# Kernel tuning notes

Measured on AMD Instinct MI355X. Metric: run time of the kernel, lower is better.

The kernel has to match this reference:

```python
import jax, jax.numpy as jnp
import numpy as np

N_NODES = 10000
N_EDGES = 640000
F_DIM = 128


def setup_inputs() -> dict:
    key = jax.random.key(0)
    k1, k2, k3, k4, k5 = jax.random.split(key, 5)
    x = jax.random.normal(k1, (N_NODES, F_DIM), dtype=jnp.float32)
    W = jax.random.uniform(k2, (F_DIM,), dtype=jnp.float32)
    edge_weight = jax.random.uniform(k3, (N_EDGES,), dtype=jnp.float32)
    edge_src = jax.random.randint(k4, (N_EDGES,), 0, N_NODES, dtype=jnp.int32)
    edge_dst = jax.random.randint(k5, (N_EDGES,), 0, N_NODES, dtype=jnp.int32)
    return {"x": x, "W": W, "edge_weight": edge_weight,
            "edge_src": edge_src, "edge_dst": edge_dst}


def reference(x, W, edge_weight, edge_src, edge_dst):
    # x @ diag(W) is just an elementwise column scale (no FxF materialization)
    xs = x * W[None, :]                                  # [N, F]
    # adj @ xs with adj given as a weighted edge list:
    # out[d] = sum_{e: dst[e]=d} edge_weight[e] * xs[src[e]]
    msgs = xs[edge_src] * edge_weight[:, None]           # [E, F] gather-scale
    out = jax.ops.segment_sum(msgs, edge_dst, num_segments=N_NODES)  # [N, F]
    return out
```

## Files before the change

### kernel.cpp

```cpp
#include <hip/hip_runtime.h>


#define F_DIM 128
#define NB 256
#define TILE 4096
#define SORT_T 512
#define NT_MAX 512
#define NH_MAX 32
#define CAPC 160

__device__ __forceinline__ unsigned f2bf_bits(float f)
{
    unsigned u = __float_as_uint(f);
    return (u + 0x7FFFu + ((u >> 16) & 1u)) >> 16;
}

__global__ void __launch_bounds__(SORT_T)
conv_sort1_kernel(const float* __restrict__ x, const float* __restrict__ W,
                  unsigned* __restrict__ xb,
                  const int* __restrict__ src, const int* __restrict__ dst,
                  const float* __restrict__ ew,
                  unsigned* __restrict__ tab, uint2* __restrict__ segs,
                  int NU4, int NT, int E, unsigned M, int R)
{
    __shared__ unsigned reo_lo[TILE];
    __shared__ unsigned reo_hi[TILE];
    __shared__ int hist[NB], scn[NB], wsum[8];

    int tid = threadIdx.x;

    if ((int)blockIdx.x >= NT) {
        int t = ((int)blockIdx.x - NT) * SORT_T + tid;
        if (t < NU4) {
            int n = t >> 4, jq = t & 15;
            const float4* xr = (const float4*)(x + (size_t)n * F_DIM + jq * 4);
            float4 a  = xr[0];
            float4 bb = xr[16];
            const float4* wr = (const float4*)(W + jq * 4);
            float4 wa = wr[0], wb = wr[16];
            uint4 o;
            o.x = f2bf_bits(a.x * wa.x) | (f2bf_bits(bb.x * wb.x) << 16);
            o.y = f2bf_bits(a.y * wa.y) | (f2bf_bits(bb.y * wb.y) << 16);
            o.z = f2bf_bits(a.z * wa.z) | (f2bf_bits(bb.z * wb.z) << 16);
            o.w = f2bf_bits(a.w * wa.w) | (f2bf_bits(bb.w * wb.w) << 16);
            *(uint4*)(xb + (size_t)n * 64 + jq * 4) = o;
        }
        return;
    }

    int tile  = (int)blockIdx.x;
    int tile0 = tile * TILE;
    int tcnt  = E - tile0; if (tcnt > TILE) tcnt = TILE;

    if (tid < NB) hist[tid] = 0;
    __syncthreads();

    int b_k[8], rank_k[8]; unsigned lo_k[8], w_k[8];
    #pragma unroll
    for (int k = 0; k < 8; ++k) {
        int e = tile0 + k * SORT_T + tid;
        b_k[k] = -1; rank_k[k] = 0; lo_k[k] = 0; w_k[k] = 0;
        if (e < E) {
            int d = dst[e];
            int b = (int)__umulhi((unsigned)d, M);
            int dl = d - b * R;
            b_k[k]    = b;
            lo_k[k]   = ((unsigned)src[e] & 0x3FFFu) | ((unsigned)dl << 14)
                      | ((unsigned)b << 21);
            w_k[k]    = __float_as_uint(ew[e]);
            rank_k[k] = atomicAdd(&hist[b], 1);
        }
    }
    __syncthreads();

    {
        int lane6 = tid & 63, wv = tid >> 6;
        int v = (tid < NB) ? hist[tid] : 0;
        #pragma unroll
        for (int d = 1; d < 64; d <<= 1) {
            int t2 = __shfl_up(v, d);
            if (lane6 >= d) v += t2;
        }
        if (lane6 == 63) wsum[wv] = v;
        __syncthreads();
        if (tid < NB) {
            int woff = 0;
            #pragma unroll
            for (int i2 = 0; i2 < 4; ++i2) if (i2 < wv) woff += wsum[i2];
            scn[tid] = v + woff;
        }
        __syncthreads();
    }

    #pragma unroll
    for (int k = 0; k < 8; ++k) {
        if (b_k[k] >= 0) {
            int b = b_k[k];
            int pos = (scn[b] - hist[b]) + rank_k[k];
            reo_lo[pos] = lo_k[k];
            reo_hi[pos] = w_k[k];
        }
    }
    __syncthreads();

    if (tid < NB)
        tab[(size_t)tid * NT_MAX + tile] =
            ((unsigned)(scn[tid] - hist[tid]) << 16) | (unsigned)hist[tid];

    for (int p = tid; p < tcnt; p += SORT_T)
        segs[(size_t)tile * TILE + p] = make_uint2(reo_lo[p], reo_hi[p]);
}

__global__ void __launch_bounds__(512)
bucket_kernel(const unsigned* __restrict__ xb, const unsigned* __restrict__ tab,
              const uint2* __restrict__ segs, float* __restrict__ out,
              int N, int R, int NT)
{
    __shared__ __align__(16) float          w_l[NH_MAX * CAPC];
    __shared__ __align__(16) unsigned short s_l[NH_MAX * CAPC];
    __shared__ unsigned tabrow[NT_MAX];
    __shared__ int cur[NH_MAX];
    __shared__ int ovf_flag;

    int blk = blockIdx.x;
    int b   = blk >> 1;
    int jh  = blk & 1;
    int tid = threadIdx.x;

    int NHALF = (R + 1) >> 1;
    int brow0 = b * R;
    int rows  = N - brow0; if (rows > R) rows = R;
    if (rows <= 0) return;
    int nlo = jh * NHALF;
    int nh  = rows - nlo; if (nh > NHALF) nh = NHALF;
    if (nh <= 0) return;

    for (int t = tid; t < NT; t += 512) tabrow[t] = tab[(size_t)b * NT_MAX + t];
    if (tid < NH_MAX) cur[tid] = tid * CAPC;
    if (tid == 0) ovf_flag = 0;
    __syncthreads();

    int wid = tid >> 6, lane = tid & 63;
    int sub = lane >> 4, l16 = lane & 15;

    for (int t = wid * 4 + sub; t < NT; t += 32) {
        unsigned e = tabrow[t];
        int c_t = (int)(e & 0xFFFFu);
        const uint2* chunk = segs + (size_t)t * TILE + (e >> 16);
        for (int l = l16; l < c_t; l += 16) {
            uint2 q = chunk[l];
            int dll = (int)((q.x >> 14) & 0x7Fu) - nlo;
            if (dll >= 0 && dll < nh) {
                int pos = atomicAdd(&cur[dll], 1);
                if (pos < dll * CAPC + CAPC) {
                    s_l[pos] = (unsigned short)(q.x & 0x3FFFu);
                    w_l[pos] = __uint_as_float(q.y);
                } else {
                    ovf_flag = 1;
                }
            }
        }
    }
    __syncthreads();

    if (!ovf_flag) {
        if (tid < nh) {
            int cnt = cur[tid] - tid * CAPC;
            int hp  = (cnt + 7) & ~7;
            for (int p = tid * CAPC + cnt; p < tid * CAPC + hp; ++p) {
                s_l[p] = 0; w_l[p] = 0.f;
            }
        }
        __syncthreads();

        #pragma unroll
        for (int j = 0; j < 4; ++j) {
            int dll = wid + j * 8;
            if (dll < nh) {
                int cnt = cur[dll] - dll * CAPC;
                int hp  = (cnt + 7) & ~7;
                int bs  = dll * CAPC;
                float ax = 0.f, ay = 0.f;
                for (int i = 0; i < hp; i += 8) {
                    uint4 sa = *(const uint4*)(s_l + bs + i);
                    float4 wa = *(const float4*)(w_l + bs + i);
                    float4 wb = *(const float4*)(w_l + bs + i + 4);
                    unsigned sv[8] = {sa.x & 0xFFFFu, sa.x >> 16,
                                      sa.y & 0xFFFFu, sa.y >> 16,
                                      sa.z & 0xFFFFu, sa.z >> 16,
                                      sa.w & 0xFFFFu, sa.w >> 16};
                    float wv[8] = {wa.x, wa.y, wa.z, wa.w,
                                   wb.x, wb.y, wb.z, wb.w};
                    unsigned rv[8];
                    #pragma unroll
                    for (int k = 0; k < 8; ++k)
                        rv[k] = xb[(size_t)sv[k] * 64 + lane];
                    #pragma unroll
                    for (int k = 0; k < 8; ++k) {
                        ax += wv[k] * __uint_as_float(rv[k] << 16);
                        ay += wv[k] * __uint_as_float(rv[k] & 0xFFFF0000u);
                    }
                }
                int n = brow0 + nlo + dll;
                out[(size_t)n * F_DIM + lane]      = ax;
                out[(size_t)n * F_DIM + 64 + lane] = ay;
            }
        }
    } else {
        #pragma unroll
        for (int j = 0; j < 4; ++j) {
            int dll = wid + j * 8;
            if (dll < nh) {
                int dwant = dll + nlo;
                float ax = 0.f, ay = 0.f;
                for (int t = 0; t < NT; ++t) {
                    unsigned e = tabrow[t];
                    int c_t = (int)(e & 0xFFFFu);
                    const uint2* chunk = segs + (size_t)t * TILE + (e >> 16);
                    for (int l = 0; l < c_t; ++l) {
                        uint2 q = chunk[l];
                        if ((int)((q.x >> 14) & 0x7Fu) == dwant) {
                            unsigned rv = xb[(size_t)(q.x & 0x3FFFu) * 64 + lane];
                            float w = __uint_as_float(q.y);
                            ax += w * __uint_as_float(rv << 16);
                            ay += w * __uint_as_float(rv & 0xFFFF0000u);
                        }
                    }
                }
                int n = brow0 + nlo + dll;
                out[(size_t)n * F_DIM + lane]      = ax;
                out[(size_t)n * F_DIM + 64 + lane] = ay;
            }
        }
    }
}

__global__ void __launch_bounds__(256)
fallback_scatter(const float* __restrict__ x, const float* __restrict__ W,
                 const float* __restrict__ ew, const int* __restrict__ src,
                 const int* __restrict__ dst, float* __restrict__ out, int E)
{
    int t = blockIdx.x * 256 + threadIdx.x;
    int e = t >> 5;
    if (e >= E) return;
    int f4 = t & 31;
    int   s = src[e];
    int   d = dst[e];
    float w = ew[e];
    float4 xv = reinterpret_cast<const float4*>(x)[s * 32 + f4];
    float4 wv = reinterpret_cast<const float4*>(W)[f4];
    float* o = out + d * F_DIM + f4 * 4;
    unsafeAtomicAdd(o + 0, xv.x * wv.x * w);
    unsafeAtomicAdd(o + 1, xv.y * wv.y * w);
    unsafeAtomicAdd(o + 2, xv.z * wv.z * w);
    unsafeAtomicAdd(o + 3, xv.w * wv.w * w);
}

extern "C" void kernel_launch(void* const* d_in, const int* in_sizes, int n_in,
                              void* d_out, int out_size, void* d_ws, size_t ws_size,
                              hipStream_t stream)
{
    const float* x   = (const float*)d_in[0];
    const float* W   = (const float*)d_in[1];
    const float* ew  = (const float*)d_in[2];
    const int*   src = (const int*)d_in[3];
    const int*   dst = (const int*)d_in[4];
    float*       out = (float*)d_out;

    const int E  = in_sizes[2];
    const int N  = out_size / F_DIM;
    const int NU = N * 64;

    const int R  = (N + NB - 1) / NB;
    const int NT = (E + TILE - 1) / TILE;

    size_t xb_off   = 0;
    size_t tab_off  = xb_off + (size_t)NU;
    size_t segs_off = tab_off + (size_t)NB * NT_MAX;
    size_t need     = (segs_off + (size_t)NT * TILE * 2) * 4;

    if (ws_size >= need && N >= 1 && N <= 16384 && NT <= NT_MAX && R <= 64) {
        unsigned* xb   = (unsigned*)d_ws + xb_off;
        unsigned* tab  = (unsigned*)d_ws + tab_off;
        uint2*    segs = (uint2*)((unsigned*)d_ws + segs_off);

        const unsigned M = (unsigned)((0x100000000ULL + R - 1) / (unsigned)R);

        int NU4    = NU / 4;
        int cgrid  = (NU4 + SORT_T - 1) / SORT_T;
        int nbuck  = (N + R - 1) / R;
        int bgrid  = 2 * nbuck;

        conv_sort1_kernel<<<NT + cgrid, SORT_T, 0, stream>>>(
            x, W, xb, src, dst, ew, tab, segs, NU4, NT, E, M, R);
        bucket_kernel<<<bgrid, 512, 0, stream>>>(xb, tab, segs, out, N, R, NT);
    } else {
        hipMemsetAsync(out, 0, (size_t)out_size * sizeof(float), stream);
        long long tt = (long long)E * 32;
        int grid = (int)((tt + 255) / 256);
        if (grid < 1) grid = 1;
        fallback_scatter<<<grid, 256, 0, stream>>>(x, W, ew, src, dst, out, E);
    }
}
```

Baseline: 32.24 us.

## Double bucket count so each bucket block reads only its own rows

Raises the destination bucket count from 256 to 512 so each bucket covers about 20 rows. The bucket kernel then uses one block per bucket instead of two half-buckets that each scanned every edge of the bucket and threw half away, which removes the duplicated segment reads and filtering. Shared-memory records are packed as one uint2 (src, weight) instead of two separate arrays. The cost is a larger histogram and tab table in the sort kernel, fewer edges per bucket per tile, and dependence on R fitting in NH_MAX (32) rows.

```diff
diff --git a/kernel.cpp b/kernel.cpp
--- a/kernel.cpp
+++ b/kernel.cpp
@@ -2,7 +2,7 @@
 
 
 #define F_DIM 128
-#define NB 256
+#define NB 512
 #define TILE 4096
 #define SORT_T 512
 #define NT_MAX 512
@@ -52,7 +52,7 @@
     int tile0 = tile * TILE;
     int tcnt  = E - tile0; if (tcnt > TILE) tcnt = TILE;
 
-    if (tid < NB) hist[tid] = 0;
+    hist[tid] = 0;
     __syncthreads();
 
     int b_k[8], rank_k[8]; unsigned lo_k[8], w_k[8];
@@ -66,7 +66,7 @@
             int dl = d - b * R;
             b_k[k]    = b;
             lo_k[k]   = ((unsigned)src[e] & 0x3FFFu) | ((unsigned)dl << 14)
-                      | ((unsigned)b << 21);
+                      | ((unsigned)b << 19);
             w_k[k]    = __float_as_uint(ew[e]);
             rank_k[k] = atomicAdd(&hist[b], 1);
         }
@@ -75,7 +75,7 @@
 
     {
         int lane6 = tid & 63, wv = tid >> 6;
-        int v = (tid < NB) ? hist[tid] : 0;
+        int v = hist[tid];
         #pragma unroll
         for (int d = 1; d < 64; d <<= 1) {
             int t2 = __shfl_up(v, d);
@@ -83,12 +83,10 @@
         }
         if (lane6 == 63) wsum[wv] = v;
         __syncthreads();
-        if (tid < NB) {
-            int woff = 0;
-            #pragma unroll
-            for (int i2 = 0; i2 < 4; ++i2) if (i2 < wv) woff += wsum[i2];
-            scn[tid] = v + woff;
-        }
+        int woff = 0;
+        #pragma unroll
+        for (int i2 = 0; i2 < 8; ++i2) if (i2 < wv) woff += wsum[i2];
+        scn[tid] = v + woff;
         __syncthreads();
     }
 
@@ -103,9 +101,8 @@
     }
     __syncthreads();
 
-    if (tid < NB)
-        tab[(size_t)tid * NT_MAX + tile] =
-            ((unsigned)(scn[tid] - hist[tid]) << 16) | (unsigned)hist[tid];
+    tab[(size_t)tid * NT_MAX + tile] =
+        ((unsigned)(scn[tid] - hist[tid]) << 16) | (unsigned)hist[tid];
 
     for (int p = tid; p < tcnt; p += SORT_T)
         segs[(size_t)tile * TILE + p] = make_uint2(reo_lo[p], reo_hi[p]);
@@ -116,24 +113,17 @@
               const uint2* __restrict__ segs, float* __restrict__ out,
               int N, int R, int NT)
 {
-    __shared__ __align__(16) float          w_l[NH_MAX * CAPC];
-    __shared__ __align__(16) unsigned short s_l[NH_MAX * CAPC];
+    __shared__ __align__(16) uint2 rec_l[NH_MAX * CAPC];
     __shared__ unsigned tabrow[NT_MAX];
     __shared__ int cur[NH_MAX];
     __shared__ int ovf_flag;
 
-    int blk = blockIdx.x;
-    int b   = blk >> 1;
-    int jh  = blk & 1;
+    int b   = blockIdx.x;
     int tid = threadIdx.x;
 
-    int NHALF = (R + 1) >> 1;
     int brow0 = b * R;
     int rows  = N - brow0; if (rows > R) rows = R;
     if (rows <= 0) return;
-    int nlo = jh * NHALF;
-    int nh  = rows - nlo; if (nh > NHALF) nh = NHALF;
-    if (nh <= 0) return;
 
     for (int t = tid; t < NT; t += 512) tabrow[t] = tab[(size_t)b * NT_MAX + t];
     if (tid < NH_MAX) cur[tid] = tid * CAPC;
@@ -141,56 +131,53 @@
     __syncthreads();
 
     int wid = tid >> 6, lane = tid & 63;
-    int sub = lane >> 4, l16 = lane & 15;
-
-    for (int t = wid * 4 + sub; t < NT; t += 32) {
+    int sub = lane >> 3, l8 = lane & 7;
+
+    for (int t = wid * 8 + sub; t < NT; t += 64) {
         unsigned e = tabrow[t];
         int c_t = (int)(e & 0xFFFFu);
         const uint2* chunk = segs + (size_t)t * TILE + (e >> 16);
-        for (int l = l16; l < c_t; l += 16) {
+        for (int l = l8; l < c_t; l += 8) {
             uint2 q = chunk[l];
-            int dll = (int)((q.x >> 14) & 0x7Fu) - nlo;
-            if (dll >= 0 && dll < nh) {
-                int pos = atomicAdd(&cur[dll], 1);
-                if (pos < dll * CAPC + CAPC) {
-                    s_l[pos] = (unsigned short)(q.x & 0x3FFFu);
-                    w_l[pos] = __uint_as_float(q.y);
-                } else {
-                    ovf_flag = 1;
-                }
+            int dll = (int)((q.x >> 14) & 0x1Fu);
+            int pos = atomicAdd(&cur[dll], 1);
+            if (pos < dll * CAPC + CAPC) {
+                rec_l[pos] = make_uint2(q.x & 0x3FFFu, q.y);
+            } else {
+                ovf_flag = 1;
             }
         }
     }
     __syncthreads();
 
     if (!ovf_flag) {
-        if (tid < nh) {
+        if (tid < rows) {
             int cnt = cur[tid] - tid * CAPC;
             int hp  = (cnt + 7) & ~7;
-            for (int p = tid * CAPC + cnt; p < tid * CAPC + hp; ++p) {
-                s_l[p] = 0; w_l[p] = 0.f;
-            }
+            for (int p = tid * CAPC + cnt; p < tid * CAPC + hp; ++p)
+                rec_l[p] = make_uint2(0u, 0u);
         }
         __syncthreads();
 
         #pragma unroll
         for (int j = 0; j < 4; ++j) {
             int dll = wid + j * 8;
-            if (dll < nh) {
+            if (dll < rows) {
                 int cnt = cur[dll] - dll * CAPC;
                 int hp  = (cnt + 7) & ~7;
-                int bs  = dll * CAPC;
+                const uint2* pr = rec_l + dll * CAPC;
                 float ax = 0.f, ay = 0.f;
                 for (int i = 0; i < hp; i += 8) {
-                    uint4 sa = *(const uint4*)(s_l + bs + i);
-                    float4 wa = *(const float4*)(w_l + bs + i);
-                    float4 wb = *(const float4*)(w_l + bs + i + 4);
-                    unsigned sv[8] = {sa.x & 0xFFFFu, sa.x >> 16,
-                                      sa.y & 0xFFFFu, sa.y >> 16,
-                                      sa.z & 0xFFFFu, sa.z >> 16,
-                                      sa.w & 0xFFFFu, sa.w >> 16};
-                    float wv[8] = {wa.x, wa.y, wa.z, wa.w,
-                                   wb.x, wb.y, wb.z, wb.w};
+                    uint4 qa = *(const uint4*)(pr + i);
+                    uint4 qb = *(const uint4*)(pr + i + 2);
+                    uint4 qc = *(const uint4*)(pr + i + 4);
+                    uint4 qd = *(const uint4*)(pr + i + 6);
+                    unsigned sv[8] = {qa.x, qa.z, qb.x, qb.z,
+                                      qc.x, qc.z, qd.x, qd.z};
+                    float wv[8] = {__uint_as_float(qa.y), __uint_as_float(qa.w),
+                                   __uint_as_float(qb.y), __uint_as_float(qb.w),
+                                   __uint_as_float(qc.y), __uint_as_float(qc.w),
+                                   __uint_as_float(qd.y), __uint_as_float(qd.w)};
                     unsigned rv[8];
                     #pragma unroll
                     for (int k = 0; k < 8; ++k)
@@ -201,7 +188,7 @@
                         ay += wv[k] * __uint_as_float(rv[k] & 0xFFFF0000u);
                     }
                 }
-                int n = brow0 + nlo + dll;
+                int n = brow0 + dll;
                 out[(size_t)n * F_DIM + lane]      = ax;
                 out[(size_t)n * F_DIM + 64 + lane] = ay;
             }
@@ -210,8 +197,7 @@
         #pragma unroll
         for (int j = 0; j < 4; ++j) {
             int dll = wid + j * 8;
-            if (dll < nh) {
-                int dwant = dll + nlo;
+            if (dll < rows) {
                 float ax = 0.f, ay = 0.f;
                 for (int t = 0; t < NT; ++t) {
                     unsigned e = tabrow[t];
@@ -219,7 +205,7 @@
                     const uint2* chunk = segs + (size_t)t * TILE + (e >> 16);
                     for (int l = 0; l < c_t; ++l) {
                         uint2 q = chunk[l];
-                        if ((int)((q.x >> 14) & 0x7Fu) == dwant) {
+                        if ((int)((q.x >> 14) & 0x1Fu) == dll) {
                             unsigned rv = xb[(size_t)(q.x & 0x3FFFu) * 64 + lane];
                             float w = __uint_as_float(q.y);
                             ax += w * __uint_as_float(rv << 16);
@@ -227,7 +213,7 @@
                         }
                     }
                 }
-                int n = brow0 + nlo + dll;
+                int n = brow0 + dll;
                 out[(size_t)n * F_DIM + lane]      = ax;
                 out[(size_t)n * F_DIM + 64 + lane] = ay;
             }
@@ -279,7 +265,7 @@
     size_t segs_off = tab_off + (size_t)NB * NT_MAX;
     size_t need     = (segs_off + (size_t)NT * TILE * 2) * 4;
 
-    if (ws_size >= need && N >= 1 && N <= 16384 && NT <= NT_MAX && R <= 64) {
+    if (ws_size >= need && N >= 1 && N <= 16384 && NT <= NT_MAX && R <= NH_MAX) {
         unsigned* xb   = (unsigned*)d_ws + xb_off;
         unsigned* tab  = (unsigned*)d_ws + tab_off;
         uint2*    segs = (uint2*)((unsigned*)d_ws + segs_off);
@@ -289,11 +275,10 @@
         int NU4    = NU / 4;
         int cgrid  = (NU4 + SORT_T - 1) / SORT_T;
         int nbuck  = (N + R - 1) / R;
-        int bgrid  = 2 * nbuck;
 
         conv_sort1_kernel<<<NT + cgrid, SORT_T, 0, stream>>>(
             x, W, xb, src, dst, ew, tab, segs, NU4, NT, E, M, R);
-        bucket_kernel<<<bgrid, 512, 0, stream>>>(xb, tab, segs, out, N, R, NT);
+        bucket_kernel<<<nbuck, 512, 0, stream>>>(xb, tab, segs, out, N, R, NT);
     } else {
         hipMemsetAsync(out, 0, (size_t)out_size * sizeof(float), stream);
         long long tt = (long long)E * 32;
```

After: 31.63 us. About the same (-1.9%).
